# Optimization experiments

Measured on AMD Instinct MI355X. Metric: run time of the kernel, lower is better.

The kernel has to match this reference:

```python
import jax, jax.numpy as jnp
import numpy as np

D_PAIR, C, N_HEAD = 128, 32, 4
B, N = 1, 256
MASK_INF = 1e9


def layernorm(x, w, b, eps=1e-5):
    mu = jnp.mean(x, axis=-1, keepdims=True)
    var = jnp.var(x, axis=-1, keepdims=True)
    return (x - mu) * jax.lax.rsqrt(var + eps) * w + b


def setup_inputs() -> dict:
    key = jax.random.key(0)
    ks = jax.random.split(key, 10)
    d, h, c = D_PAIR, N_HEAD, C
    s = 0.02
    return {
        "Z_raw": jax.random.normal(ks[0], (B, N, N, d), jnp.float32),
        "Z_mask": jnp.ones((B, N, N), jnp.float32),
        "ln_w": jnp.ones((d,), jnp.float32),
        "ln_b": jnp.zeros((d,), jnp.float32),
        "w_b": jax.random.normal(ks[1], (d, h), jnp.float32) * s,   # pair-bias proj, no bias
        "wq": jax.random.normal(ks[2], (d, h, c), jnp.float32) * s,
        "wk": jax.random.normal(ks[3], (d, h, c), jnp.float32) * s,
        "wv": jax.random.normal(ks[4], (d, h, c), jnp.float32) * s,
        "wg": jax.random.normal(ks[5], (d, h, c), jnp.float32) * s,
        "bg": jnp.ones((h, c), jnp.float32),                        # AF2 gating bias init = 1
        "wo": jax.random.normal(ks[6], (h, c, d), jnp.float32) * s, # last_bias_fuse: no bias here
        "out_bias": jnp.zeros((d,), jnp.float32),
    }


def reference(Z_raw, Z_mask, ln_w, ln_b, w_b, wq, wk, wv, wg, bg, wo, out_bias):
    # Z_raw: [B, I, J, d] pair tensor; attention over J for each row I.
    Z = layernorm(Z_raw, ln_w, ln_b)
    # triangle bias: [B, I, J, h] -> broadcast per-head bias [B, 1, h, q, k]
    tri_b = jnp.einsum("bqkd,dh->bhqk", Z, w_b)[:, None]
    # mask bias over key dim: [B, I, 1, 1, K]
    mask_b = (MASK_INF * (Z_mask - 1.0))[:, :, None, None, :]
    scale = C ** -0.5
    q = jnp.einsum("bijd,dhc->bijhc", Z, wq) * scale
    k = jnp.einsum("bijd,dhc->bijhc", Z, wk)
    v = jnp.einsum("bijd,dhc->bijhc", Z, wv)
    logits = jnp.einsum("biqhc,bikhc->bihqk", q, k) + mask_b + tri_b
    a = jax.nn.softmax(logits, axis=-1)
    o = jnp.einsum("bihqk,bikhc->biqhc", a, v)
    g = jax.nn.sigmoid(jnp.einsum("bijd,dhc->bijhc", Z, wg) + bg)
    o = o * g
    out = jnp.einsum("biqhc,hcd->biqd", o, wo)
    # bias_dropout_add with all-ones dropout mask, inference mode -> plain add
    return out + out_bias + Z_raw
```

## Files before the change

kernel.cpp:

```cpp
#include <hip/hip_runtime.h>


#define NDIM 256
#define HDIM 4
#define QK_SCALE 0.17677669529663687f

typedef unsigned short u16;
typedef unsigned int u32;
typedef __attribute__((ext_vector_type(8))) short bf16x8;
typedef __attribute__((ext_vector_type(4))) float f32x4;

__device__ __forceinline__ float bf2f_lo(u32 u){ union {u32 i; float f;} v; v.i = u<<16; return v.f; }
__device__ __forceinline__ float bf2f_hi(u32 u){ union {u32 i; float f;} v; v.i = u & 0xffff0000u; return v.f; }
__device__ __forceinline__ float bf2f(u16 u){ union {u32 i; float f;} v; v.i = ((u32)u)<<16; return v.f; }
__device__ __forceinline__ u16 f2bf(float f){
    union {u32 i; float f;} v; v.f = f;
    u32 r = v.i + 0x7fffu + ((v.i>>16)&1u);
    return (u16)(r>>16);
}
__device__ __forceinline__ u32 pack2(float a, float b){ return ((u32)f2bf(a)) | (((u32)f2bf(b))<<16); }

template<bool BF16> __device__ __forceinline__ float ld1(const void* p, long i){
    if (BF16) return bf2f(((const u16*)p)[i]);
    return ((const float*)p)[i];
}
template<bool BF16> __device__ __forceinline__ float2 ld2f(const void* p, long pair){
    if (BF16){ u32 u = ((const u32*)p)[pair]; return make_float2(bf2f_lo(u), bf2f_hi(u)); }
    return ((const float2*)p)[pair];
}
template<bool BF16> __device__ __forceinline__ void st1(void* p, long i, float v){
    if (BF16) ((u16*)p)[i] = f2bf(v);
    else      ((float*)p)[i] = v;
}
template<bool BF16> __device__ __forceinline__ void load8f(const void* p, long idx, float* f){
    if (BF16){
        uint4 u = *(const uint4*)((const u16*)p + idx);
        f[0]=bf2f_lo(u.x); f[1]=bf2f_hi(u.x); f[2]=bf2f_lo(u.y); f[3]=bf2f_hi(u.y);
        f[4]=bf2f_lo(u.z); f[5]=bf2f_hi(u.z); f[6]=bf2f_lo(u.w); f[7]=bf2f_hi(u.w);
    } else {
        const float4* q = (const float4*)((const float*)p + idx);
        float4 a = q[0], b = q[1];
        f[0]=a.x; f[1]=a.y; f[2]=a.z; f[3]=a.w; f[4]=b.x; f[5]=b.y; f[6]=b.z; f[7]=b.w;
    }
}
__device__ __forceinline__ bf16x8 pack8(const float* f){
    bf16x8 r;
    #pragma unroll
    for (int j = 0; j < 8; j++) r[j] = (short)f2bf(f[j]);
    return r;
}
__device__ __forceinline__ void unpack16(uint4 u, u16* e){
    e[0]=(u16)u.x; e[1]=(u16)(u.x>>16); e[2]=(u16)u.y; e[3]=(u16)(u.y>>16);
    e[4]=(u16)u.z; e[5]=(u16)(u.z>>16); e[6]=(u16)u.w; e[7]=(u16)(u.w>>16);
}
__device__ __forceinline__ bool mask_is_bf16(const void* mask){
    return ((const u32*)mask)[0] == 0x3F803F80u;
}

template<bool BF16>
__global__ __launch_bounds__(256, 2) void proj_kernel(
    const void* __restrict__ zraw, const void* __restrict__ mask,
    const void* __restrict__ lnw, const void* __restrict__ lnb,
    const void* __restrict__ wb,
    const void* __restrict__ wq, const void* __restrict__ wk,
    const void* __restrict__ wv, const void* __restrict__ wg,
    const void* __restrict__ bg,
    u16* __restrict__ trib,
    u16* __restrict__ qb, u16* __restrict__ kb,
    u16* __restrict__ vb, u16* __restrict__ gb)
{
    if (mask_is_bf16(mask) != BF16) return;
    __shared__ u16 zA[128*136];
    __shared__ u16 wS[128*136];
    __shared__ u16 wbS[16*136];
    __shared__ float muS[128], rsS[128], lnS[128], lbS[128];
    int t = threadIdx.x, w = t >> 6, L = t & 63, lm = L & 15, lq = L >> 4;
    int pos0 = blockIdx.x * 128;
    int i = pos0 >> 8, j0 = pos0 & 255;

    if (t < 128){ lnS[t] = ld1<BF16>(lnw, t); lbS[t] = ld1<BF16>(lnb, t); }
    for (int idx = t; idx < 16*136; idx += 256) wbS[idx] = 0;
    if (BF16){
        const uint4* zp = (const uint4*)((const u16*)zraw + (long)pos0*128);
        #pragma unroll
        for (int n = 0; n < 8; n++){
            int g = t + n*256;
            int row = g >> 4, c0 = (g & 15)*8;
            *(uint4*)&zA[row*136 + c0] = zp[g];
        }
    } else {
        const float4* zp = (const float4*)((const float*)zraw + (long)pos0*128);
        #pragma unroll
        for (int n = 0; n < 16; n++){
            int g = t + n*256;
            int row = g >> 5, c0 = (g & 31)*4;
            float4 f = zp[g];
            *(u32*)&zA[row*136 + c0]     = pack2(f.x, f.y);
            *(u32*)&zA[row*136 + c0 + 2] = pack2(f.z, f.w);
        }
    }
    __syncthreads();
    {
        int row = t >> 1, half = t & 1;
        float s = 0.f, ss = 0.f;
        #pragma unroll
        for (int n = 0; n < 8; n++){
            bf16x8 v = *(const bf16x8*)&zA[row*136 + half*64 + n*8];
            #pragma unroll
            for (int j = 0; j < 8; j++){ float x = bf2f((u16)v[j]); s += x; ss += x*x; }
        }
        s += __shfl_xor(s, 1); ss += __shfl_xor(ss, 1);
        if (half == 0){
            float mu = s*(1.f/128.f);
            float var = ss*(1.f/128.f) - mu*mu;
            muS[row] = mu; rsS[row] = rsqrtf(var + 1e-5f);
        }
    }
    for (int idx = t; idx < 512; idx += 256){
        int d = idx >> 2, n = idx & 3;
        wbS[n*136 + d] = f2bf(ld1<BF16>(wb, idx));
    }
    __syncthreads();
    #pragma unroll 8
    for (int n = 0; n < 64; n++){
        int e = t + n*256;
        int row = e >> 7, col = e & 127;
        float x = bf2f(zA[row*136 + col]);
        zA[row*136 + col] = f2bf((x - muS[row])*rsS[row]*lnS[col] + lbS[col]);
    }
    __syncthreads();
    bf16x8 aA[2][4];
    #pragma unroll
    for (int Mt = 0; Mt < 2; Mt++)
        #pragma unroll
        for (int ks = 0; ks < 4; ks++)
            aA[Mt][ks] = *(const bf16x8*)&zA[((2*w + Mt)*16 + lm)*136 + ks*32 + lq*8];
    f32x4 zero = {0.f,0.f,0.f,0.f};
    {
        bf16x8 bB[4];
        #pragma unroll
        for (int ks = 0; ks < 4; ks++)
            bB[ks] = *(const bf16x8*)&wbS[lm*136 + ks*32 + lq*8];
        #pragma unroll
        for (int Mt = 0; Mt < 2; Mt++){
            f32x4 a = zero;
            #pragma unroll
            for (int ks = 0; ks < 4; ks++)
                a = __builtin_amdgcn_mfma_f32_16x16x32_bf16(aA[Mt][ks], bB[ks], a, 0, 0, 0);
            if (lm < 4){
                #pragma unroll
                for (int r = 0; r < 4; r++){
                    int row = (2*w + Mt)*16 + lq*4 + r;
                    trib[((long)(lm*NDIM + i))*NDIM + j0 + row] = f2bf(a[r]);
                }
            }
        }
    }
    const void* Ws[4] = {wq, wk, wv, wg};
    u16* Os[4] = {qb, kb, vb, gb};
    for (int m = 0; m < 4; m++){
        __syncthreads();
        if (BF16){
            const uint4* wp = (const uint4*)Ws[m];
            #pragma unroll
            for (int n = 0; n < 8; n++){
                int g = t + n*256;
                int d = g >> 4, n0 = (g & 15)*8;
                u16 e[8]; unpack16(wp[g], e);
                #pragma unroll
                for (int q2 = 0; q2 < 8; q2++) wS[(n0 + q2)*136 + d] = e[q2];
            }
        } else {
            const float* wp = (const float*)Ws[m];
            #pragma unroll
            for (int n = 0; n < 64; n++){
                int g = t + n*256;
                int d = g >> 7, nc = g & 127;
                wS[nc*136 + d] = f2bf(wp[g]);
            }
        }
        __syncthreads();
        f32x4 acc[2][8];
        #pragma unroll
        for (int Mt = 0; Mt < 2; Mt++)
            #pragma unroll
            for (int Nt = 0; Nt < 8; Nt++) acc[Mt][Nt] = zero;
        #pragma unroll
        for (int ks = 0; ks < 4; ks++){
            bf16x8 bB[8];
            #pragma unroll
            for (int Nt = 0; Nt < 8; Nt++)
                bB[Nt] = *(const bf16x8*)&wS[(Nt*16 + lm)*136 + ks*32 + lq*8];
            #pragma unroll
            for (int Mt = 0; Mt < 2; Mt++)
                #pragma unroll
                for (int Nt = 0; Nt < 8; Nt++)
                    acc[Mt][Nt] = __builtin_amdgcn_mfma_f32_16x16x32_bf16(aA[Mt][ks], bB[Nt], acc[Mt][Nt], 0, 0, 0);
        }
        u16* outp = Os[m];
        #pragma unroll
        for (int Nt = 0; Nt < 8; Nt++){
            int n = Nt*16 + lm;
            int hh = n >> 5, c = n & 31;
            float bgv = (m == 3) ? ld1<BF16>(bg, n) : 0.f;
            #pragma unroll
            for (int Mt = 0; Mt < 2; Mt++)
                #pragma unroll
                for (int r = 0; r < 4; r++){
                    float v = acc[Mt][Nt][r];
                    if (m == 0) v *= QK_SCALE;
                    if (m == 3) v = 1.f/(1.f + __expf(-(v + bgv)));
                    int row = (2*w + Mt)*16 + lq*4 + r;
                    outp[((long)(i*HDIM + hh)*NDIM + (j0 + row))*32 + c] = f2bf(v);
                }
        }
    }
}

template<bool BF16>
__global__ __launch_bounds__(256, 2) void attn_kernel(
    const void* __restrict__ mask,
    const u16* __restrict__ qb, const u16* __restrict__ kb,
    const u16* __restrict__ vb, const u16* __restrict__ gb,
    const u16* __restrict__ trib, u16* __restrict__ obuf)
{
    if (mask_is_bf16(mask) != BF16) return;
    __shared__ u16 kS[256*40];
    __shared__ u16 vS[32*264];
    __shared__ u16 pT[4][32*72];
    __shared__ float mrow[256];
    int b = blockIdx.x;
    int i = b >> 3, h = (b >> 1) & 3, half = b & 1;
    int t = threadIdx.x, w = t >> 6, L = t & 63, lm = L & 15, lq = L >> 4;
    long base = (long)(i*HDIM + h)*NDIM*32;

    const uint4* kp = (const uint4*)(kb + base);
    const uint4* vp = (const uint4*)(vb + base);
    #pragma unroll
    for (int n = 0; n < 4; n++){
        int g = t + n*256;
        int j = g >> 2, c0 = (g & 3)*8;
        *(uint4*)&kS[j*40 + c0] = kp[g];
        u16 e[8]; unpack16(vp[g], e);
        #pragma unroll
        for (int q2 = 0; q2 < 8; q2++)
            vS[(j >> 3)*264 + (c0 + q2)*8 + (j & 7)] = e[q2];
    }
    mrow[t] = 1e9f*(ld1<BF16>(mask, i*NDIM + t) - 1.f);
    int q0 = half*128 + w*32;
    bf16x8 qA[2];
    #pragma unroll
    for (int Mt = 0; Mt < 2; Mt++)
        qA[Mt] = *(const bf16x8*)(qb + base + (long)(q0 + Mt*16 + lm)*32 + lq*8);
    __syncthreads();

    const u16* trq = trib + (long)h*NDIM*NDIM;
    f32x4 zero = {0.f,0.f,0.f,0.f};
    u32 Spk[2][4][8];
    float mS[2][4];
    #pragma unroll
    for (int Mt = 0; Mt < 2; Mt++)
        #pragma unroll
        for (int r = 0; r < 4; r++) mS[Mt][r] = -3e38f;

    u16 trc[2][4][2], trn[2][4][2];
    #pragma unroll
    for (int Mt = 0; Mt < 2; Mt++)
        #pragma unroll
        for (int r = 0; r < 4; r++)
            #pragma unroll
            for (int hf = 0; hf < 2; hf++)
                trc[Mt][r][hf] = trq[(long)(q0 + Mt*16 + lq*4 + r)*NDIM + hf*16 + lm];
    for (int kt = 0; kt < 8; kt++){
        if (kt < 7){
            #pragma unroll
            for (int Mt = 0; Mt < 2; Mt++)
                #pragma unroll
                for (int r = 0; r < 4; r++)
                    #pragma unroll
                    for (int hf = 0; hf < 2; hf++)
                        trn[Mt][r][hf] = trq[(long)(q0 + Mt*16 + lq*4 + r)*NDIM + (kt+1)*32 + hf*16 + lm];
        }
        bf16x8 kB0 = *(const bf16x8*)&kS[(kt*32 + lm)*40 + lq*8];
        bf16x8 kB1 = *(const bf16x8*)&kS[(kt*32 + 16 + lm)*40 + lq*8];
        float mb0 = mrow[kt*32 + lm], mb1 = mrow[kt*32 + 16 + lm];
        #pragma unroll
        for (int Mt = 0; Mt < 2; Mt++){
            f32x4 S0 = __builtin_amdgcn_mfma_f32_16x16x32_bf16(qA[Mt], kB0, zero, 0, 0, 0);
            f32x4 S1 = __builtin_amdgcn_mfma_f32_16x16x32_bf16(qA[Mt], kB1, zero, 0, 0, 0);
            #pragma unroll
            for (int r = 0; r < 4; r++){
                float x0 = S0[r] + mb0 + bf2f(trc[Mt][r][0]);
                float x1 = S1[r] + mb1 + bf2f(trc[Mt][r][1]);
                mS[Mt][r] = fmaxf(mS[Mt][r], fmaxf(x0, x1));
                Spk[Mt][r][kt] = pack2(x0, x1);
            }
        }
        #pragma unroll
        for (int Mt = 0; Mt < 2; Mt++)
            #pragma unroll
            for (int r = 0; r < 4; r++){
                trc[Mt][r][0] = trn[Mt][r][0];
                trc[Mt][r][1] = trn[Mt][r][1];
            }
    }
    #pragma unroll
    for (int Mt = 0; Mt < 2; Mt++)
        #pragma unroll
        for (int r = 0; r < 4; r++){
            float m = mS[Mt][r];
            #pragma unroll
            for (int off = 1; off <= 8; off <<= 1) m = fmaxf(m, __shfl_xor(m, off));
            mS[Mt][r] = m;
        }

    float lsum[2][4] = {{0.f,0.f,0.f,0.f},{0.f,0.f,0.f,0.f}};
    f32x4 O[2][2];
    O[0][0] = zero; O[0][1] = zero; O[1][0] = zero; O[1][1] = zero;
    u16* myp = pT[w];
    #pragma unroll
    for (int ch = 0; ch < 4; ch++){
        #pragma unroll
        for (int Mt = 0; Mt < 2; Mt++)
            #pragma unroll
            for (int r = 0; r < 4; r++){
                int qr = Mt*16 + lq*4 + r;
                #pragma unroll
                for (int kk = 0; kk < 2; kk++){
                    u32 sp = Spk[Mt][r][ch*2 + kk];
                    float p0 = __expf(bf2f_lo(sp) - mS[Mt][r]);
                    float p1 = __expf(bf2f_hi(sp) - mS[Mt][r]);
                    lsum[Mt][r] += p0 + p1;
                    myp[qr*72 + kk*32 + lm]      = f2bf(p0);
                    myp[qr*72 + kk*32 + 16 + lm] = f2bf(p1);
                }
            }
        #pragma unroll
        for (int ks = 0; ks < 2; ks++){
            int kbi = ch*8 + ks*4 + lq;
            bf16x8 vB0 = *(const bf16x8*)&vS[kbi*264 + lm*8];
            bf16x8 vB1 = *(const bf16x8*)&vS[kbi*264 + (16 + lm)*8];
            #pragma unroll
            for (int Mt = 0; Mt < 2; Mt++){
                bf16x8 pA = *(const bf16x8*)&myp[(Mt*16 + lm)*72 + ks*32 + lq*8];
                O[Mt][0] = __builtin_amdgcn_mfma_f32_16x16x32_bf16(pA, vB0, O[Mt][0], 0, 0, 0);
                O[Mt][1] = __builtin_amdgcn_mfma_f32_16x16x32_bf16(pA, vB1, O[Mt][1], 0, 0, 0);
            }
        }
    }
    #pragma unroll
    for (int Mt = 0; Mt < 2; Mt++)
        #pragma unroll
        for (int r = 0; r < 4; r++){
            float l = lsum[Mt][r];
            #pragma unroll
            for (int off = 1; off <= 8; off <<= 1) l += __shfl_xor(l, off);
            lsum[Mt][r] = l;
        }
    #pragma unroll
    for (int Mt = 0; Mt < 2; Mt++)
        #pragma unroll
        for (int r = 0; r < 4; r++){
            float inv = 1.f/lsum[Mt][r];
            int q = q0 + Mt*16 + lq*4 + r;
            long ob = (long)(i*NDIM + q)*128 + h*32;
            obuf[ob + lm]      = f2bf(O[Mt][0][r]*inv*bf2f(gb[base + (long)q*32 + lm]));
            obuf[ob + 16 + lm] = f2bf(O[Mt][1][r]*inv*bf2f(gb[base + (long)q*32 + 16 + lm]));
        }
}

template<bool BF16>
__global__ __launch_bounds__(256, 2) void outproj_mfma_kernel(
    const void* __restrict__ mask, const u16* __restrict__ obuf,
    const void* __restrict__ wo, const void* __restrict__ obias,
    const void* __restrict__ zraw, void* __restrict__ out)
{
    if (mask_is_bf16(mask) != BF16) return;
    __shared__ u16 woT[128*136];
    int t = threadIdx.x, w = t >> 6, L = t & 63;
    int lm = L & 15, lq = L >> 4;
    for (int idx = t; idx < 16384; idx += 256){
        int hc = idx >> 7, d = idx & 127;
        woT[d*136 + hc] = f2bf(ld1<BF16>(wo, (long)hc*128 + d));
    }
    __syncthreads();
    int pos0 = blockIdx.x*128 + w*32;
    bf16x8 aA[2][4];
    #pragma unroll
    for (int Mt = 0; Mt < 2; Mt++)
        #pragma unroll
        for (int ks = 0; ks < 4; ks++)
            aA[Mt][ks] = *(const bf16x8*)&obuf[((long)(pos0 + Mt*16 + lm))*128 + ks*32 + lq*8];
    f32x4 zero = {0.f,0.f,0.f,0.f};
    f32x4 acc[2][8];
    #pragma unroll
    for (int Mt = 0; Mt < 2; Mt++)
        #pragma unroll
        for (int Nt = 0; Nt < 8; Nt++) acc[Mt][Nt] = zero;
    #pragma unroll
    for (int ks = 0; ks < 4; ks++){
        bf16x8 bB[8];
        #pragma unroll
        for (int Nt = 0; Nt < 8; Nt++)
            bB[Nt] = *(const bf16x8*)&woT[(Nt*16 + lm)*136 + ks*32 + lq*8];
        #pragma unroll
        for (int Mt = 0; Mt < 2; Mt++)
            #pragma unroll
            for (int Nt = 0; Nt < 8; Nt++)
                acc[Mt][Nt] = __builtin_amdgcn_mfma_f32_16x16x32_bf16(aA[Mt][ks], bB[Nt], acc[Mt][Nt], 0, 0, 0);
    }
    float ob[8];
    #pragma unroll
    for (int Nt = 0; Nt < 8; Nt++) ob[Nt] = ld1<BF16>(obias, Nt*16 + lm);
    #pragma unroll
    for (int Mt = 0; Mt < 2; Mt++)
        #pragma unroll
        for (int Nt = 0; Nt < 8; Nt++)
            #pragma unroll
            for (int r = 0; r < 4; r++){
                long pos = pos0 + Mt*16 + lq*4 + r;
                int d = Nt*16 + lm;
                float v = acc[Mt][Nt][r] + ob[Nt] + ld1<BF16>(zraw, pos*128 + d);
                st1<BF16>(out, pos*128 + d, v);
            }
}

template<bool BF16>
__global__ __launch_bounds__(256) void ln_tri_kernel(
    const void* __restrict__ zraw, const void* __restrict__ mask,
    const void* __restrict__ lnw, const void* __restrict__ lnb,
    const void* __restrict__ wb, u16* __restrict__ trib)
{
    if (mask_is_bf16(mask) != BF16) return;
    int wave = threadIdx.x >> 6;
    int lane = threadIdx.x & 63;
    int pos = blockIdx.x * 4 + wave;
    float2 f = ld2f<BF16>(zraw, (long)pos*64 + lane);
    float x0 = f.x, x1 = f.y;
    float s = x0 + x1, ss = x0*x0 + x1*x1;
    #pragma unroll
    for (int off = 32; off; off >>= 1){ s += __shfl_xor(s, off); ss += __shfl_xor(ss, off); }
    float mean = s * (1.0f/128.0f);
    float var  = ss * (1.0f/128.0f) - mean*mean;
    float rstd = rsqrtf(var + 1e-5f);
    int d0 = lane*2;
    float y0 = (x0 - mean)*rstd*ld1<BF16>(lnw, d0)   + ld1<BF16>(lnb, d0);
    float y1 = (x1 - mean)*rstd*ld1<BF16>(lnw, d0+1) + ld1<BF16>(lnb, d0+1);
    int i = pos >> 8, j = pos & 255;
    #pragma unroll
    for (int hh = 0; hh < 4; hh++){
        float tp = y0*ld1<BF16>(wb, d0*4 + hh) + y1*ld1<BF16>(wb, (d0+1)*4 + hh);
        #pragma unroll
        for (int off = 32; off; off >>= 1) tp += __shfl_xor(tp, off);
        if (lane == 0) trib[((long)(hh*NDIM + i))*NDIM + j] = f2bf(tp);
    }
}

template<bool BF16>
__global__ __launch_bounds__(256, 2) void attn_mfma_kernel(
    const void* __restrict__ zraw, const void* __restrict__ mask,
    const void* __restrict__ lnw, const void* __restrict__ lnb,
    const void* __restrict__ wq, const void* __restrict__ wk,
    const void* __restrict__ wv, const void* __restrict__ wg,
    const void* __restrict__ bg, const u16* __restrict__ trib,
    u16* __restrict__ obuf)
{
    if (mask_is_bf16(mask) != BF16) return;
    __shared__ u16 wT[32*136];
    __shared__ u16 kS[256*40];
    __shared__ u16 vT[32*264];
    __shared__ u16 pT[4*64*40];
    __shared__ float mrow[256];
    __shared__ float lnS[128], lbS[128];

    int i = blockIdx.x >> 2, h = blockIdx.x & 3;
    int t = threadIdx.x, w = t >> 6, L = t & 63;
    int lm = L & 15, lq = L >> 4;
    mrow[t] = 1e9f*(ld1<BF16>(mask, i*NDIM + t) - 1.0f);
    if (t < 128) lnS[t] = ld1<BF16>(lnw, t);
    else         lbS[t-128] = ld1<BF16>(lnb, t-128);
    __syncthreads();

    int q0 = w*64;
    float zf[4][4][8];
    float s[4] = {0,0,0,0}, ss[4] = {0,0,0,0};
    #pragma unroll
    for (int Mt = 0; Mt < 4; Mt++){
        long row = (long)(i*NDIM + q0 + Mt*16 + lm);
        #pragma unroll
        for (int ks = 0; ks < 4; ks++){
            load8f<BF16>(zraw, row*128 + ks*32 + lq*8, zf[Mt][ks]);
            #pragma unroll
            for (int j = 0; j < 8; j++){ float x = zf[Mt][ks][j]; s[Mt] += x; ss[Mt] += x*x; }
        }
    }
    #pragma unroll
    for (int Mt = 0; Mt < 4; Mt++){
        s[Mt]  += __shfl_xor(s[Mt], 16);  s[Mt]  += __shfl_xor(s[Mt], 32);
        ss[Mt] += __shfl_xor(ss[Mt], 16); ss[Mt] += __shfl_xor(ss[Mt], 32);
    }
    bf16x8 zA[4][4];
    #pragma unroll
    for (int Mt = 0; Mt < 4; Mt++){
        float mean = s[Mt]*(1.f/128.f);
        float var  = ss[Mt]*(1.f/128.f) - mean*mean;
        float rstd = rsqrtf(var + 1e-5f);
        #pragma unroll
        for (int ks = 0; ks < 4; ks++){
            float tmp[8];
            #pragma unroll
            for (int j = 0; j < 8; j++){
                int col = ks*32 + lq*8 + j;
                tmp[j] = (zf[Mt][ks][j] - mean)*rstd*lnS[col] + lbS[col];
            }
            zA[Mt][ks] = pack8(tmp);
        }
    }
    u16* myp = pT + w*2560;
    f32x4 zero = {0.f, 0.f, 0.f, 0.f};
    auto stageW = [&](const void* W){
        for (int idx = t; idx < 4096; idx += 256){
            int c = idx >> 7, d = idx & 127;
            wT[c*136 + d] = f2bf(ld1<BF16>(W, (long)(d*4 + h)*32 + c));
        }
    };
    auto projA = [&](f32x4 (&acc)[4][2]){
        bf16x8 bB[2][4];
        #pragma unroll
        for (int Nt = 0; Nt < 2; Nt++)
            #pragma unroll
            for (int ks = 0; ks < 4; ks++)
                bB[Nt][ks] = *(const bf16x8*)&wT[(Nt*16 + lm)*136 + ks*32 + lq*8];
        #pragma unroll
        for (int Mt = 0; Mt < 4; Mt++)
            #pragma unroll
            for (int Nt = 0; Nt < 2; Nt++){
                f32x4 a = zero;
                #pragma unroll
                for (int ks = 0; ks < 4; ks++)
                    a = __builtin_amdgcn_mfma_f32_16x16x32_bf16(zA[Mt][ks], bB[Nt][ks], a, 0, 0, 0);
                acc[Mt][Nt] = a;
            }
    };
    f32x4 acc[4][2];
    stageW(wq); __syncthreads();
    projA(acc);
    #pragma unroll
    for (int Mt = 0; Mt < 4; Mt++)
        #pragma unroll
        for (int Nt = 0; Nt < 2; Nt++)
            #pragma unroll
            for (int r = 0; r < 4; r++)
                myp[(Mt*16 + lq*4 + r)*40 + Nt*16 + lm] = f2bf(acc[Mt][Nt][r]*QK_SCALE);
    bf16x8 qA[4];
    #pragma unroll
    for (int Mt = 0; Mt < 4; Mt++)
        qA[Mt] = *(const bf16x8*)&myp[(Mt*16 + lm)*40 + lq*8];
    __syncthreads();
    stageW(wk); __syncthreads();
    projA(acc);
    #pragma unroll
    for (int Mt = 0; Mt < 4; Mt++)
        #pragma unroll
        for (int Nt = 0; Nt < 2; Nt++)
            #pragma unroll
            for (int r = 0; r < 4; r++)
                kS[(q0 + Mt*16 + lq*4 + r)*40 + Nt*16 + lm] = f2bf(acc[Mt][Nt][r]);
    __syncthreads();
    stageW(wv); __syncthreads();
    projA(acc);
    #pragma unroll
    for (int Mt = 0; Mt < 4; Mt++)
        #pragma unroll
        for (int Nt = 0; Nt < 2; Nt++)
            #pragma unroll
            for (int r = 0; r < 4; r++)
                vT[(Nt*16 + lm)*264 + q0 + Mt*16 + lq*4 + r] = f2bf(acc[Mt][Nt][r]);
    __syncthreads();
    stageW(wg); __syncthreads();
    f32x4 gv[4][2];
    projA(gv);
    float bgv0 = ld1<BF16>(bg, h*32 + lm), bgv1 = ld1<BF16>(bg, h*32 + 16 + lm);
    #pragma unroll
    for (int Mt = 0; Mt < 4; Mt++)
        #pragma unroll
        for (int r = 0; r < 4; r++){
            gv[Mt][0][r] = 1.f/(1.f + __expf(-(gv[Mt][0][r] + bgv0)));
            gv[Mt][1][r] = 1.f/(1.f + __expf(-(gv[Mt][1][r] + bgv1)));
        }
    __syncthreads();
    float mS[4][4], lS[4][4];
    f32x4 O[4][2];
    #pragma unroll
    for (int Mt = 0; Mt < 4; Mt++){
        #pragma unroll
        for (int r = 0; r < 4; r++){ mS[Mt][r] = -3e38f; lS[Mt][r] = 0.f; }
        O[Mt][0] = zero; O[Mt][1] = zero;
    }
    const u16* trb = trib + ((long)(h*NDIM + q0))*NDIM;
    for (int kt = 0; kt < 8; kt++){
        bf16x8 kB0 = *(const bf16x8*)&kS[(kt*32 + lm)*40 + lq*8];
        bf16x8 kB1 = *(const bf16x8*)&kS[(kt*32 + 16 + lm)*40 + lq*8];
        f32x4 S[4][2];
        #pragma unroll
        for (int Mt = 0; Mt < 4; Mt++){
            S[Mt][0] = __builtin_amdgcn_mfma_f32_16x16x32_bf16(qA[Mt], kB0, zero, 0, 0, 0);
            S[Mt][1] = __builtin_amdgcn_mfma_f32_16x16x32_bf16(qA[Mt], kB1, zero, 0, 0, 0);
        }
        int k0 = kt*32 + lm;
        float mb0 = mrow[k0], mb1 = mrow[k0 + 16];
        #pragma unroll
        for (int Mt = 0; Mt < 4; Mt++){
            #pragma unroll
            for (int r = 0; r < 4; r++){
                int qrow = Mt*16 + lq*4 + r;
                float x0 = S[Mt][0][r] + mb0 + bf2f(trb[(long)qrow*NDIM + k0]);
                float x1 = S[Mt][1][r] + mb1 + bf2f(trb[(long)qrow*NDIM + k0 + 16]);
                float mx = fmaxf(x0, x1);
                #pragma unroll
                for (int off = 1; off <= 8; off <<= 1) mx = fmaxf(mx, __shfl_xor(mx, off));
                float mnew = fmaxf(mS[Mt][r], mx);
                float al = __expf(mS[Mt][r] - mnew);
                float p0 = __expf(x0 - mnew), p1 = __expf(x1 - mnew);
                float rs = p0 + p1;
                #pragma unroll
                for (int off = 1; off <= 8; off <<= 1) rs += __shfl_xor(rs, off);
                lS[Mt][r] = lS[Mt][r]*al + rs;
                mS[Mt][r] = mnew;
                O[Mt][0][r] *= al; O[Mt][1][r] *= al;
                myp[qrow*40 + lm]      = f2bf(p0);
                myp[qrow*40 + 16 + lm] = f2bf(p1);
            }
        }
        bf16x8 vB0 = *(const bf16x8*)&vT[lm*264 + kt*32 + lq*8];
        bf16x8 vB1 = *(const bf16x8*)&vT[(16 + lm)*264 + kt*32 + lq*8];
        #pragma unroll
        for (int Mt = 0; Mt < 4; Mt++){
            bf16x8 pA = *(const bf16x8*)&myp[(Mt*16 + lm)*40 + lq*8];
            O[Mt][0] = __builtin_amdgcn_mfma_f32_16x16x32_bf16(pA, vB0, O[Mt][0], 0, 0, 0);
            O[Mt][1] = __builtin_amdgcn_mfma_f32_16x16x32_bf16(pA, vB1, O[Mt][1], 0, 0, 0);
        }
    }
    #pragma unroll
    for (int Mt = 0; Mt < 4; Mt++)
        #pragma unroll
        for (int r = 0; r < 4; r++){
            float inv = 1.0f/lS[Mt][r];
            int q = q0 + Mt*16 + lq*4 + r;
            long base = ((long)(i*NDIM + q))*128 + h*32;
            obuf[base + lm]      = f2bf(O[Mt][0][r]*inv*gv[Mt][0][r]);
            obuf[base + 16 + lm] = f2bf(O[Mt][1][r]*inv*gv[Mt][1][r]);
        }
}

extern "C" void kernel_launch(void* const* d_in, const int* in_sizes, int n_in,
                              void* d_out, int out_size, void* d_ws, size_t ws_size,
                              hipStream_t stream)
{
    const void* zraw = d_in[0];
    const void* mask = d_in[1];
    const void* lnw  = d_in[2];
    const void* lnb  = d_in[3];
    const void* wb   = d_in[4];
    const void* wq   = d_in[5];
    const void* wk   = d_in[6];
    const void* wv   = d_in[7];
    const void* wg   = d_in[8];
    const void* bg   = d_in[9];
    const void* wo   = d_in[10];
    const void* obias= d_in[11];

    const size_t MB = 1024*1024;
    u16* trib = (u16*)d_ws;
    size_t need_big = 81*MB;
    bool big = ws_size >= need_big;

    if (big){
        u16* qb   = (u16*)((char*)d_ws + 1*MB);
        u16* kb   = (u16*)((char*)d_ws + 17*MB);
        u16* vb   = (u16*)((char*)d_ws + 33*MB);
        u16* gb   = (u16*)((char*)d_ws + 49*MB);
        u16* obuf = (u16*)((char*)d_ws + 65*MB);
        proj_kernel<true ><<<dim3(512), 256, 0, stream>>>(
            zraw, mask, lnw, lnb, wb, wq, wk, wv, wg, bg, trib, qb, kb, vb, gb);
        proj_kernel<false><<<dim3(512), 256, 0, stream>>>(
            zraw, mask, lnw, lnb, wb, wq, wk, wv, wg, bg, trib, qb, kb, vb, gb);
        attn_kernel<true ><<<dim3(2048), 256, 0, stream>>>(mask, qb, kb, vb, gb, trib, obuf);
        attn_kernel<false><<<dim3(2048), 256, 0, stream>>>(mask, qb, kb, vb, gb, trib, obuf);
        outproj_mfma_kernel<true ><<<dim3(512), 256, 0, stream>>>(mask, obuf, wo, obias, zraw, d_out);
        outproj_mfma_kernel<false><<<dim3(512), 256, 0, stream>>>(mask, obuf, wo, obias, zraw, d_out);
    } else {
        u16* obuf = (u16*)((char*)d_ws + 1*MB);
        ln_tri_kernel<true ><<<dim3(NDIM*NDIM/4), 256, 0, stream>>>(zraw, mask, lnw, lnb, wb, trib);
        ln_tri_kernel<false><<<dim3(NDIM*NDIM/4), 256, 0, stream>>>(zraw, mask, lnw, lnb, wb, trib);
        attn_mfma_kernel<true ><<<dim3(NDIM*HDIM), 256, 0, stream>>>(
            zraw, mask, lnw, lnb, wq, wk, wv, wg, bg, trib, obuf);
        attn_mfma_kernel<false><<<dim3(NDIM*HDIM), 256, 0, stream>>>(
            zraw, mask, lnw, lnb, wq, wk, wv, wg, bg, trib, obuf);
        outproj_mfma_kernel<true ><<<dim3(512), 256, 0, stream>>>(mask, obuf, wo, obias, zraw, d_out);
        outproj_mfma_kernel<false><<<dim3(512), 256, 0, stream>>>(mask, obuf, wo, obias, zraw, d_out);
    }
}
```

Before: 214.9 us.

## Pre-transpose weights once in a prep kernel and read B operands from global

```diff
diff --git a/kernel.cpp b/kernel.cpp
--- a/kernel.cpp
+++ b/kernel.cpp
@@ -58,12 +58,43 @@
 }
 
 template<bool BF16>
-__global__ __launch_bounds__(256, 2) void proj_kernel(
+__global__ __launch_bounds__(256) void prep_kernel(
+    const void* __restrict__ mask,
+    const void* __restrict__ wq, const void* __restrict__ wk,
+    const void* __restrict__ wv, const void* __restrict__ wg,
+    const void* __restrict__ wb, const void* __restrict__ wo,
+    u16* __restrict__ wTall, u16* __restrict__ woT, u16* __restrict__ wbT)
+{
+    if (mask_is_bf16(mask) != BF16) return;
+    int b = blockIdx.x, t = threadIdx.x;
+    if (b < 16){
+        const void* Ws[4] = {wq, wk, wv, wg};
+        int m = b >> 2, n0 = (b & 3)*32;
+        const void* W = Ws[m];
+        for (int idx = t; idx < 32*128; idx += 256){
+            int n = n0 + (idx >> 7), d = idx & 127;
+            wTall[(long)m*16384 + n*128 + d] = f2bf(ld1<BF16>(W, (long)d*128 + n));
+        }
+    } else {
+        int d0 = (b - 16)*32;
+        for (int idx = t; idx < 32*128; idx += 256){
+            int d = d0 + (idx >> 7), hc = idx & 127;
+            woT[d*128 + hc] = f2bf(ld1<BF16>(wo, (long)hc*128 + d));
+        }
+        if (b == 16){
+            for (int idx = t; idx < 16*128; idx += 256){
+                int n = idx >> 7, d = idx & 127;
+                wbT[n*128 + d] = (n < 4) ? f2bf(ld1<BF16>(wb, (long)d*4 + n)) : (u16)0;
+            }
+        }
+    }
+}
+
+template<bool BF16>
+__global__ __launch_bounds__(256, 3) void proj_kernel(
     const void* __restrict__ zraw, const void* __restrict__ mask,
     const void* __restrict__ lnw, const void* __restrict__ lnb,
-    const void* __restrict__ wb,
-    const void* __restrict__ wq, const void* __restrict__ wk,
-    const void* __restrict__ wv, const void* __restrict__ wg,
+    const u16* __restrict__ wTall, const u16* __restrict__ wbT,
     const void* __restrict__ bg,
     u16* __restrict__ trib,
     u16* __restrict__ qb, u16* __restrict__ kb,
@@ -71,15 +102,12 @@
 {
     if (mask_is_bf16(mask) != BF16) return;
     __shared__ u16 zA[128*136];
-    __shared__ u16 wS[128*136];
-    __shared__ u16 wbS[16*136];
     __shared__ float muS[128], rsS[128], lnS[128], lbS[128];
     int t = threadIdx.x, w = t >> 6, L = t & 63, lm = L & 15, lq = L >> 4;
     int pos0 = blockIdx.x * 128;
     int i = pos0 >> 8, j0 = pos0 & 255;
 
     if (t < 128){ lnS[t] = ld1<BF16>(lnw, t); lbS[t] = ld1<BF16>(lnb, t); }
-    for (int idx = t; idx < 16*136; idx += 256) wbS[idx] = 0;
     if (BF16){
         const uint4* zp = (const uint4*)((const u16*)zraw + (long)pos0*128);
         #pragma unroll
@@ -116,10 +144,6 @@
             muS[row] = mu; rsS[row] = rsqrtf(var + 1e-5f);
         }
     }
-    for (int idx = t; idx < 512; idx += 256){
-        int d = idx >> 2, n = idx & 3;
-        wbS[n*136 + d] = f2bf(ld1<BF16>(wb, idx));
-    }
     __syncthreads();
     #pragma unroll 8
     for (int n = 0; n < 64; n++){
@@ -140,7 +164,7 @@
         bf16x8 bB[4];
         #pragma unroll
         for (int ks = 0; ks < 4; ks++)
-            bB[ks] = *(const bf16x8*)&wbS[lm*136 + ks*32 + lq*8];
+            bB[ks] = *(const bf16x8*)&wbT[lm*128 + ks*32 + lq*8];
         #pragma unroll
         for (int Mt = 0; Mt < 2; Mt++){
             f32x4 a = zero;
@@ -156,30 +180,9 @@
             }
         }
     }
-    const void* Ws[4] = {wq, wk, wv, wg};
     u16* Os[4] = {qb, kb, vb, gb};
     for (int m = 0; m < 4; m++){
-        __syncthreads();
-        if (BF16){
-            const uint4* wp = (const uint4*)Ws[m];
-            #pragma unroll
-            for (int n = 0; n < 8; n++){
-                int g = t + n*256;
-                int d = g >> 4, n0 = (g & 15)*8;
-                u16 e[8]; unpack16(wp[g], e);
-                #pragma unroll
-                for (int q2 = 0; q2 < 8; q2++) wS[(n0 + q2)*136 + d] = e[q2];
-            }
-        } else {
-            const float* wp = (const float*)Ws[m];
-            #pragma unroll
-            for (int n = 0; n < 64; n++){
-                int g = t + n*256;
-                int d = g >> 7, nc = g & 127;
-                wS[nc*136 + d] = f2bf(wp[g]);
-            }
-        }
-        __syncthreads();
+        const u16* wT = wTall + (long)m*16384;
         f32x4 acc[2][8];
         #pragma unroll
         for (int Mt = 0; Mt < 2; Mt++)
@@ -190,7 +193,7 @@
             bf16x8 bB[8];
             #pragma unroll
             for (int Nt = 0; Nt < 8; Nt++)
-                bB[Nt] = *(const bf16x8*)&wS[(Nt*16 + lm)*136 + ks*32 + lq*8];
+                bB[Nt] = *(const bf16x8*)&wT[(Nt*16 + lm)*128 + ks*32 + lq*8];
             #pragma unroll
             for (int Mt = 0; Mt < 2; Mt++)
                 #pragma unroll
@@ -370,20 +373,14 @@
 }
 
 template<bool BF16>
-__global__ __launch_bounds__(256, 2) void outproj_mfma_kernel(
+__global__ __launch_bounds__(256, 3) void outproj_mfma_kernel(
     const void* __restrict__ mask, const u16* __restrict__ obuf,
-    const void* __restrict__ wo, const void* __restrict__ obias,
+    const u16* __restrict__ woT, const void* __restrict__ obias,
     const void* __restrict__ zraw, void* __restrict__ out)
 {
     if (mask_is_bf16(mask) != BF16) return;
-    __shared__ u16 woT[128*136];
     int t = threadIdx.x, w = t >> 6, L = t & 63;
     int lm = L & 15, lq = L >> 4;
-    for (int idx = t; idx < 16384; idx += 256){
-        int hc = idx >> 7, d = idx & 127;
-        woT[d*136 + hc] = f2bf(ld1<BF16>(wo, (long)hc*128 + d));
-    }
-    __syncthreads();
     int pos0 = blockIdx.x*128 + w*32;
     bf16x8 aA[2][4];
     #pragma unroll
@@ -402,7 +399,7 @@
         bf16x8 bB[8];
         #pragma unroll
         for (int Nt = 0; Nt < 8; Nt++)
-            bB[Nt] = *(const bf16x8*)&woT[(Nt*16 + lm)*136 + ks*32 + lq*8];
+            bB[Nt] = *(const bf16x8*)&woT[(Nt*16 + lm)*128 + ks*32 + lq*8];
         #pragma unroll
         for (int Mt = 0; Mt < 2; Mt++)
             #pragma unroll
@@ -653,6 +650,62 @@
         }
 }
 
+template<bool BF16>
+__global__ __launch_bounds__(256, 2) void outproj_staged_kernel(
+    const void* __restrict__ mask, const u16* __restrict__ obuf,
+    const void* __restrict__ wo, const void* __restrict__ obias,
+    const void* __restrict__ zraw, void* __restrict__ out)
+{
+    if (mask_is_bf16(mask) != BF16) return;
+    __shared__ u16 woT[128*136];
+    int t = threadIdx.x, w = t >> 6, L = t & 63;
+    int lm = L & 15, lq = L >> 4;
+    for (int idx = t; idx < 16384; idx += 256){
+        int hc = idx >> 7, d = idx & 127;
+        woT[d*136 + hc] = f2bf(ld1<BF16>(wo, (long)hc*128 + d));
+    }
+    __syncthreads();
+    int pos0 = blockIdx.x*128 + w*32;
+    bf16x8 aA[2][4];
+    #pragma unroll
+    for (int Mt = 0; Mt < 2; Mt++)
+        #pragma unroll
+        for (int ks = 0; ks < 4; ks++)
+            aA[Mt][ks] = *(const bf16x8*)&obuf[((long)(pos0 + Mt*16 + lm))*128 + ks*32 + lq*8];
+    f32x4 zero = {0.f,0.f,0.f,0.f};
+    f32x4 acc[2][8];
+    #pragma unroll
+    for (int Mt = 0; Mt < 2; Mt++)
+        #pragma unroll
+        for (int Nt = 0; Nt < 8; Nt++) acc[Mt][Nt] = zero;
+    #pragma unroll
+    for (int ks = 0; ks < 4; ks++){
+        bf16x8 bB[8];
+        #pragma unroll
+        for (int Nt = 0; Nt < 8; Nt++)
+            bB[Nt] = *(const bf16x8*)&woT[(Nt*16 + lm)*136 + ks*32 + lq*8];
+        #pragma unroll
+        for (int Mt = 0; Mt < 2; Mt++)
+            #pragma unroll
+            for (int Nt = 0; Nt < 8; Nt++)
+                acc[Mt][Nt] = __builtin_amdgcn_mfma_f32_16x16x32_bf16(aA[Mt][ks], bB[Nt], acc[Mt][Nt], 0, 0, 0);
+    }
+    float ob[8];
+    #pragma unroll
+    for (int Nt = 0; Nt < 8; Nt++) ob[Nt] = ld1<BF16>(obias, Nt*16 + lm);
+    #pragma unroll
+    for (int Mt = 0; Mt < 2; Mt++)
+        #pragma unroll
+        for (int Nt = 0; Nt < 8; Nt++)
+            #pragma unroll
+            for (int r = 0; r < 4; r++){
+                long pos = pos0 + Mt*16 + lq*4 + r;
+                int d = Nt*16 + lm;
+                float v = acc[Mt][Nt][r] + ob[Nt] + ld1<BF16>(zraw, pos*128 + d);
+                st1<BF16>(out, pos*128 + d, v);
+            }
+}
+
 extern "C" void kernel_launch(void* const* d_in, const int* in_sizes, int n_in,
                               void* d_out, int out_size, void* d_ws, size_t ws_size,
                               hipStream_t stream)
@@ -671,24 +724,29 @@
     const void* obias= d_in[11];
 
     const size_t MB = 1024*1024;
+    const size_t KB = 1024;
     u16* trib = (u16*)d_ws;
-    size_t need_big = 81*MB;
-    bool big = ws_size >= need_big;
+    bool big = ws_size >= 81*MB;
 
     if (big){
-        u16* qb   = (u16*)((char*)d_ws + 1*MB);
-        u16* kb   = (u16*)((char*)d_ws + 17*MB);
-        u16* vb   = (u16*)((char*)d_ws + 33*MB);
-        u16* gb   = (u16*)((char*)d_ws + 49*MB);
-        u16* obuf = (u16*)((char*)d_ws + 65*MB);
+        u16* wTall = (u16*)((char*)d_ws + 512*KB);
+        u16* woT   = (u16*)((char*)d_ws + 512*KB + 128*KB);
+        u16* wbT   = (u16*)((char*)d_ws + 512*KB + 160*KB);
+        u16* qb    = (u16*)((char*)d_ws + 1*MB);
+        u16* kb    = (u16*)((char*)d_ws + 17*MB);
+        u16* vb    = (u16*)((char*)d_ws + 33*MB);
+        u16* gb    = (u16*)((char*)d_ws + 49*MB);
+        u16* obuf  = (u16*)((char*)d_ws + 65*MB);
+        prep_kernel<true ><<<dim3(20), 256, 0, stream>>>(mask, wq, wk, wv, wg, wb, wo, wTall, woT, wbT);
+        prep_kernel<false><<<dim3(20), 256, 0, stream>>>(mask, wq, wk, wv, wg, wb, wo, wTall, woT, wbT);
         proj_kernel<true ><<<dim3(512), 256, 0, stream>>>(
-            zraw, mask, lnw, lnb, wb, wq, wk, wv, wg, bg, trib, qb, kb, vb, gb);
+            zraw, mask, lnw, lnb, wTall, wbT, bg, trib, qb, kb, vb, gb);
         proj_kernel<false><<<dim3(512), 256, 0, stream>>>(
-            zraw, mask, lnw, lnb, wb, wq, wk, wv, wg, bg, trib, qb, kb, vb, gb);
+            zraw, mask, lnw, lnb, wTall, wbT, bg, trib, qb, kb, vb, gb);
         attn_kernel<true ><<<dim3(2048), 256, 0, stream>>>(mask, qb, kb, vb, gb, trib, obuf);
         attn_kernel<false><<<dim3(2048), 256, 0, stream>>>(mask, qb, kb, vb, gb, trib, obuf);
-        outproj_mfma_kernel<true ><<<dim3(512), 256, 0, stream>>>(mask, obuf, wo, obias, zraw, d_out);
-        outproj_mfma_kernel<false><<<dim3(512), 256, 0, stream>>>(mask, obuf, wo, obias, zraw, d_out);
+        outproj_mfma_kernel<true ><<<dim3(512), 256, 0, stream>>>(mask, obuf, woT, obias, zraw, d_out);
+        outproj_mfma_kernel<false><<<dim3(512), 256, 0, stream>>>(mask, obuf, woT, obias, zraw, d_out);
     } else {
         u16* obuf = (u16*)((char*)d_ws + 1*MB);
         ln_tri_kernel<true ><<<dim3(NDIM*NDIM/4), 256, 0, stream>>>(zraw, mask, lnw, lnb, wb, trib);
@@ -697,7 +755,7 @@
             zraw, mask, lnw, lnb, wq, wk, wv, wg, bg, trib, obuf);
         attn_mfma_kernel<false><<<dim3(NDIM*HDIM), 256, 0, stream>>>(
             zraw, mask, lnw, lnb, wq, wk, wv, wg, bg, trib, obuf);
-        outproj_mfma_kernel<true ><<<dim3(512), 256, 0, stream>>>(mask, obuf, wo, obias, zraw, d_out);
-        outproj_mfma_kernel<false><<<dim3(512), 256, 0, stream>>>(mask, obuf, wo, obias, zraw, d_out);
-    }
-}
+        outproj_staged_kernel<true ><<<dim3(512), 256, 0, stream>>>(mask, obuf, wo, obias, zraw, d_out);
+        outproj_staged_kernel<false><<<dim3(512), 256, 0, stream>>>(mask, obuf, wo, obias, zraw, d_out);
+    }
+}
```

Result: slower. 224.2 us (+4.3%).
